# Kernel tuning notes

Measured on AMD Instinct MI355X. Metric: run time of the kernel, lower is better.

The kernel has to match this reference:

```python
import jax, jax.numpy as jnp
import numpy as np

N, IN_SIZE, OUT_SIZE = 8192, 256, 64


def setup_inputs() -> dict:
    key = jax.random.key(0)
    kx, kw, kb = jax.random.split(key, 3)
    x = jax.random.normal(kx, (N, IN_SIZE), dtype=jnp.float32)
    # Per-feature Linear(1, out_size): weight w[i] (shape [out_size]) and bias b[i].
    # torch.nn.Linear(1, out_size) init: U(-1, 1) since fan_in = 1.
    W = jax.random.uniform(kw, (IN_SIZE, OUT_SIZE), minval=-1.0, maxval=1.0, dtype=jnp.float32)
    b = jax.random.uniform(kb, (IN_SIZE, OUT_SIZE), minval=-1.0, maxval=1.0, dtype=jnp.float32)
    return {"x": x, "W": W, "b": b}


def reference(x, W, b):
    # x: [N, F]; W, b: [F, D]
    # layer_i(x[:, i:i+1]) = x[:, i, None] * W[i] + b[i]  -> stacked [N, D, F] in torch,
    # here [N, F, D]; mean over feature axis is identical either way.
    out = x[:, :, None] * W[None, :, :] + b[None, :, :]  # [N, F, D]
    out = jnp.nan_to_num(out)
    return out.mean(axis=1)  # [N, D]
```

## Files before the change

### kernel.cpp

```cpp
#include <hip/hip_runtime.h>
#include <stdint.h>

#define NROWS 8192
#define FDIM  256
#define DDIM  64

constexpr int RPB = 64;
constexpr int CPB = 32;
constexpr int XS  = 258;

__device__ inline unsigned int pack2_bf16_rne(float a, float b) {
    unsigned int ua = __float_as_uint(a);
    unsigned int ub = __float_as_uint(b);
    ua += 0x7fffu + ((ua >> 16) & 1u);
    ub += 0x7fffu + ((ub >> 16) & 1u);
    return (ua >> 16) | (ub & 0xffff0000u);
}

__global__ __launch_bounds__(256)
void nanembed_kernel(const float* __restrict__ x,
                     const float* __restrict__ W,
                     const float* __restrict__ b,
                     float* __restrict__ out)
{
    __shared__ __align__(16) unsigned short xs[RPB * XS];
    __shared__ float bias_part[8][32];
    __shared__ float bm[32];

    const int tid  = threadIdx.x;
    const int lane = tid & 63;
    const int wave = tid >> 6;
    const int wu   = __builtin_amdgcn_readfirstlane(wave);
    const int row0 = blockIdx.x * RPB;
    const int c0   = blockIdx.y * CPB;

    {
        const float4* xv4 = reinterpret_cast<const float4*>(x + (size_t)row0 * FDIM);
        #pragma unroll
        for (int i = 0; i < 16; ++i) {
            int idx = tid + i * 256;
            int r   = idx >> 6;
            int s   = idx & 63;
            float4 v = xv4[idx];
            unsigned int u0 = pack2_bf16_rne(v.x, v.y);
            unsigned int u1 = pack2_bf16_rne(v.z, v.w);
            unsigned int* dst = reinterpret_cast<unsigned int*>(&xs[r * XS + s * 4]);
            dst[0] = u0;
            dst[1] = u1;
        }
    }

    {
        const int c  = tid & 31;
        const int fs = tid >> 5;
        float s = 0.f;
        #pragma unroll 8
        for (int k = 0; k < 32; ++k)
            s += b[(size_t)(fs * 32 + k) * DDIM + c0 + c];
        bias_part[fs][c] = s;
    }

    __syncthreads();

    float acc[CPB];
    #pragma unroll
    for (int c = 0; c < CPB; ++c) acc[c] = 0.f;

    const int fbase = wu * 64;
    const float* __restrict__ Wb = W + (size_t)fbase * DDIM + c0;
    const unsigned short* xrow = &xs[lane * XS + fbase];

    #pragma unroll 4
    for (int f2 = 0; f2 < 32; ++f2) {
        unsigned int uw = *reinterpret_cast<const unsigned int*>(xrow + 2 * f2);
        float xlo = __uint_as_float(uw << 16);
        float xhi = __uint_as_float(uw & 0xffff0000u);
        const float* w0 = Wb + (size_t)(2 * f2) * DDIM;
        const float* w1 = Wb + (size_t)(2 * f2 + 1) * DDIM;
        #pragma unroll
        for (int c = 0; c < CPB; ++c) acc[c] = fmaf(xlo, w0[c], acc[c]);
        #pragma unroll
        for (int c = 0; c < CPB; ++c) acc[c] = fmaf(xhi, w1[c], acc[c]);
    }

    __syncthreads();

    float* pbuf = reinterpret_cast<float*>(xs);
    #pragma unroll
    for (int c = 0; c < CPB; ++c)
        pbuf[(wu * CPB + c) * 64 + lane] = acc[c];

    if (tid < CPB) {
        float s = 0.f;
        #pragma unroll
        for (int k = 0; k < 8; ++k) s += bias_part[k][tid];
        bm[tid] = s;
    }

    __syncthreads();

    {
        const int r  = tid >> 2;
        const int cb = (tid & 3) * 8;
        float4 o[2];
        float* of = reinterpret_cast<float*>(o);
        #pragma unroll
        for (int j = 0; j < 8; ++j) {
            const int c = cb + j;
            float s = bm[c];
            #pragma unroll
            for (int w = 0; w < 4; ++w)
                s += pbuf[(w * CPB + c) * 64 + r];
            of[j] = s * (1.0f / 256.0f);
        }
        float4* op = reinterpret_cast<float4*>(out + (size_t)(row0 + r) * DDIM + c0 + cb);
        op[0] = o[0];
        op[1] = o[1];
    }
}

extern "C" void kernel_launch(void* const* d_in, const int* in_sizes, int n_in,
                              void* d_out, int out_size, void* d_ws, size_t ws_size,
                              hipStream_t stream) {
    const float* x = (const float*)d_in[0];
    const float* W = (const float*)d_in[1];
    const float* b = (const float*)d_in[2];
    float* out = (float*)d_out;

    dim3 grid(NROWS / RPB, DDIM / CPB);
    nanembed_kernel<<<grid, 256, 0, stream>>>(x, W, b, out);
}
```

Before: 71.04 us.

## Replace scalar FMA GEMV-style kernel with bf16 MFMA 16x16x32 kernel

Rewrites the kernel so that x@W is computed with bf16 MFMA instructions. Each block now handles 32 rows and all 64 output columns with two waves. x fragments are loaded straight from global memory into registers and converted to bf16. W is converted into bf16 B-fragments and stored in LDS by every block. This removes the scalar FMA loop, the LDS staging of x and the cross-wave reduction. In exchange, W conversion and the bias sum are repeated in each of 256 blocks, and the output is written with scalar strided stores.

```diff
diff --git a/kernel.cpp b/kernel.cpp
--- a/kernel.cpp
+++ b/kernel.cpp
@@ -5,11 +5,10 @@
 #define FDIM  256
 #define DDIM  64
 
-constexpr int RPB = 64;
-constexpr int CPB = 32;
-constexpr int XS  = 258;
+typedef __attribute__((ext_vector_type(8))) short short8;
+typedef __attribute__((ext_vector_type(4))) float floatx4;
 
-__device__ inline unsigned int pack2_bf16_rne(float a, float b) {
+__device__ inline unsigned int pack2_bf16(float a, float b) {
     unsigned int ua = __float_as_uint(a);
     unsigned int ub = __float_as_uint(b);
     ua += 0x7fffu + ((ua >> 16) & 1u);
@@ -17,105 +16,92 @@
     return (ua >> 16) | (ub & 0xffff0000u);
 }
 
-__global__ __launch_bounds__(256)
-void nanembed_kernel(const float* __restrict__ x,
-                     const float* __restrict__ W,
-                     const float* __restrict__ b,
-                     float* __restrict__ out)
+__global__ __launch_bounds__(128)
+void nanembed_mfma(const float* __restrict__ x,
+                   const float* __restrict__ W,
+                   const float* __restrict__ b,
+                   float* __restrict__ out)
 {
-    __shared__ __align__(16) unsigned short xs[RPB * XS];
-    __shared__ float bias_part[8][32];
-    __shared__ float bm[32];
+    __shared__ __align__(16) unsigned int bfrag_lds[2048 * 4];
+    __shared__ float4 bias_part[8][16];
 
     const int tid  = threadIdx.x;
     const int lane = tid & 63;
-    const int wave = tid >> 6;
-    const int wu   = __builtin_amdgcn_readfirstlane(wave);
-    const int row0 = blockIdx.x * RPB;
-    const int c0   = blockIdx.y * CPB;
+    const int w    = tid >> 6;
+    const int q    = lane >> 4;
+    const int n    = lane & 15;
+    const int r0   = blockIdx.x * 32;
 
-    {
-        const float4* xv4 = reinterpret_cast<const float4*>(x + (size_t)row0 * FDIM);
-        #pragma unroll
-        for (int i = 0; i < 16; ++i) {
-            int idx = tid + i * 256;
-            int r   = idx >> 6;
-            int s   = idx & 63;
-            float4 v = xv4[idx];
-            unsigned int u0 = pack2_bf16_rne(v.x, v.y);
-            unsigned int u1 = pack2_bf16_rne(v.z, v.w);
-            unsigned int* dst = reinterpret_cast<unsigned int*>(&xs[r * XS + s * 4]);
-            dst[0] = u0;
-            dst[1] = u1;
-        }
+    const int row = r0 + w * 16 + n;
+    const float4* xp = reinterpret_cast<const float4*>(x + (size_t)row * FDIM + q * 8);
+    float4 xv[16];
+    #pragma unroll
+    for (int ks = 0; ks < 8; ++ks) {
+        xv[2 * ks]     = xp[ks * 8];
+        xv[2 * ks + 1] = xp[ks * 8 + 1];
+    }
+
+    #pragma unroll
+    for (int i = 0; i < 16; ++i) {
+        int f  = tid + i * 128;
+        int ks = f >> 8;
+        int nt = (f >> 6) & 3;
+        int fl = f & 63;
+        int fq = fl >> 4;
+        int c  = nt * 16 + (fl & 15);
+        const float* wp = W + (size_t)(ks * 32 + fq * 8) * DDIM + c;
+        union { short8 s; unsigned int u[4]; } fr;
+        fr.u[0] = pack2_bf16(wp[0 * DDIM], wp[1 * DDIM]);
+        fr.u[1] = pack2_bf16(wp[2 * DDIM], wp[3 * DDIM]);
+        fr.u[2] = pack2_bf16(wp[4 * DDIM], wp[5 * DDIM]);
+        fr.u[3] = pack2_bf16(wp[6 * DDIM], wp[7 * DDIM]);
+        reinterpret_cast<short8*>(bfrag_lds)[f] = fr.s;
     }
 
     {
-        const int c  = tid & 31;
-        const int fs = tid >> 5;
-        float s = 0.f;
+        const int c4 = tid & 15;
+        const int h  = tid >> 4;
+        const float4* bp = reinterpret_cast<const float4*>(b) + c4;
+        float4 s = make_float4(0.f, 0.f, 0.f, 0.f);
         #pragma unroll 8
-        for (int k = 0; k < 32; ++k)
-            s += b[(size_t)(fs * 32 + k) * DDIM + c0 + c];
-        bias_part[fs][c] = s;
+        for (int f = h * 32; f < h * 32 + 32; ++f) {
+            float4 v = bp[(size_t)f * 16];
+            s.x += v.x; s.y += v.y; s.z += v.z; s.w += v.w;
+        }
+        bias_part[h][c4] = s;
     }
 
     __syncthreads();
 
-    float acc[CPB];
+    floatx4 acc[4] = {{0.f, 0.f, 0.f, 0.f}, {0.f, 0.f, 0.f, 0.f},
+                      {0.f, 0.f, 0.f, 0.f}, {0.f, 0.f, 0.f, 0.f}};
     #pragma unroll
-    for (int c = 0; c < CPB; ++c) acc[c] = 0.f;
-
-    const int fbase = wu * 64;
-    const float* __restrict__ Wb = W + (size_t)fbase * DDIM + c0;
-    const unsigned short* xrow = &xs[lane * XS + fbase];
-
-    #pragma unroll 4
-    for (int f2 = 0; f2 < 32; ++f2) {
-        unsigned int uw = *reinterpret_cast<const unsigned int*>(xrow + 2 * f2);
-        float xlo = __uint_as_float(uw << 16);
-        float xhi = __uint_as_float(uw & 0xffff0000u);
-        const float* w0 = Wb + (size_t)(2 * f2) * DDIM;
-        const float* w1 = Wb + (size_t)(2 * f2 + 1) * DDIM;
+    for (int ks = 0; ks < 8; ++ks) {
+        union { short8 s; unsigned int u[4]; } fa;
+        float4 v0 = xv[2 * ks], v1 = xv[2 * ks + 1];
+        fa.u[0] = pack2_bf16(v0.x, v0.y);
+        fa.u[1] = pack2_bf16(v0.z, v0.w);
+        fa.u[2] = pack2_bf16(v1.x, v1.y);
+        fa.u[3] = pack2_bf16(v1.z, v1.w);
         #pragma unroll
-        for (int c = 0; c < CPB; ++c) acc[c] = fmaf(xlo, w0[c], acc[c]);
-        #pragma unroll
-        for (int c = 0; c < CPB; ++c) acc[c] = fmaf(xhi, w1[c], acc[c]);
+        for (int nt = 0; nt < 4; ++nt) {
+            short8 fb = reinterpret_cast<const short8*>(bfrag_lds)[ks * 256 + nt * 64 + lane];
+            acc[nt] = __builtin_amdgcn_mfma_f32_16x16x32_bf16(fa.s, fb, acc[nt], 0, 0, 0);
+        }
     }
 
-    __syncthreads();
-
-    float* pbuf = reinterpret_cast<float*>(xs);
     #pragma unroll
-    for (int c = 0; c < CPB; ++c)
-        pbuf[(wu * CPB + c) * 64 + lane] = acc[c];
-
-    if (tid < CPB) {
-        float s = 0.f;
+    for (int nt = 0; nt < 4; ++nt) {
+        const int c = nt * 16 + n;
+        float bs = 0.f;
         #pragma unroll
-        for (int k = 0; k < 8; ++k) s += bias_part[k][tid];
-        bm[tid] = s;
-    }
-
-    __syncthreads();
-
-    {
-        const int r  = tid >> 2;
-        const int cb = (tid & 3) * 8;
-        float4 o[2];
-        float* of = reinterpret_cast<float*>(o);
+        for (int h = 0; h < 8; ++h)
+            bs += reinterpret_cast<const float*>(&bias_part[h][0])[c];
         #pragma unroll
-        for (int j = 0; j < 8; ++j) {
-            const int c = cb + j;
-            float s = bm[c];
-            #pragma unroll
-            for (int w = 0; w < 4; ++w)
-                s += pbuf[(w * CPB + c) * 64 + r];
-            of[j] = s * (1.0f / 256.0f);
+        for (int reg = 0; reg < 4; ++reg) {
+            const int r = r0 + w * 16 + q * 4 + reg;
+            out[(size_t)r * DDIM + c] = (acc[nt][reg] + bs) * (1.0f / 256.0f);
         }
-        float4* op = reinterpret_cast<float4*>(out + (size_t)(row0 + r) * DDIM + c0 + cb);
-        op[0] = o[0];
-        op[1] = o[1];
     }
 }
 
@@ -127,6 +113,5 @@
     const float* b = (const float*)d_in[2];
     float* out = (float*)d_out;
 
-    dim3 grid(NROWS / RPB, DDIM / CPB);
-    nanembed_kernel<<<grid, 256, 0, stream>>>(x, W, b, out);
+    nanembed_mfma<<<dim3(NROWS / 32), 128, 0, stream>>>(x, W, b, out);
 }
```

New measurement: 65.56 us. 7.7% less time.
